# Optimization experiments

Hardware: AMD Instinct MI355X
Metric: run time of the kernel (lower is better)

## Reference

```python
import jax, jax.numpy as jnp
import numpy as np

D_MODEL = 512
NHEAD = 8
HEAD_DIM = D_MODEL // NHEAD
DFF = 2048
KSIZE = 3
EPS = 1e-5


def conv1d(x, w, b, pad):
    # x: [B, Cin, S], w: [Cout, Cin, K] -> [B, Cout, S]
    y = jax.lax.conv_general_dilated(x, w, window_strides=(1,), padding=[(pad, pad)],
                                     dimension_numbers=("NCH", "OIH", "NCH"))
    return y + b[None, :, None]


def layernorm(x, g, b):
    mu = jnp.mean(x, axis=-1, keepdims=True)
    var = jnp.mean(jnp.square(x - mu), axis=-1, keepdims=True)
    return (x - mu) * jax.lax.rsqrt(var + EPS) * g + b


def setup_inputs() -> dict:
    key = jax.random.key(0)
    ks = jax.random.split(key, 16)
    B, S = 8, 1024
    # conv init: normal(0, sqrt(2/(K*out_ch))) per head (out_ch = HEAD_DIM), bias 0.1
    sq = np.sqrt(2.0 / (KSIZE * HEAD_DIM)).astype(np.float32)
    sv = np.sqrt(2.0 / (1 * HEAD_DIM)).astype(np.float32)
    inp = {
        "src": jax.random.normal(ks[0], (B, S, D_MODEL), jnp.float32),
        "Wq": jax.random.normal(ks[1], (D_MODEL, D_MODEL, KSIZE), jnp.float32) * sq,
        "bq": jnp.full((D_MODEL,), 0.1, jnp.float32),
        "Wk": jax.random.normal(ks[2], (D_MODEL, D_MODEL, KSIZE), jnp.float32) * sq,
        "bk": jnp.full((D_MODEL,), 0.1, jnp.float32),
        "Wv": jax.random.normal(ks[3], (D_MODEL, D_MODEL, 1), jnp.float32) * sv,
        "bv": jnp.full((D_MODEL,), 0.1, jnp.float32),
        "Wo": jax.random.normal(ks[4], (D_MODEL, D_MODEL), jnp.float32) * 0.02,
        "bo": jnp.zeros((D_MODEL,), jnp.float32),
        "W1": jax.random.normal(ks[5], (DFF, D_MODEL), jnp.float32) * 0.02,
        "b1": jnp.zeros((DFF,), jnp.float32),
        "W2": jax.random.normal(ks[6], (D_MODEL, DFF), jnp.float32) * 0.02,
        "b2": jnp.zeros((D_MODEL,), jnp.float32),
        "g1": jnp.ones((D_MODEL,), jnp.float32),
        "be1": jnp.zeros((D_MODEL,), jnp.float32),
        "g2": jnp.ones((D_MODEL,), jnp.float32),
        "be2": jnp.zeros((D_MODEL,), jnp.float32),
    }
    return inp


def reference(src, Wq, bq, Wk, bk, Wv, bv, Wo, bo, W1, b1, W2, b2, g1, be1, g2, be2):
    B, S, D = src.shape
    H, hd = NHEAD, HEAD_DIM
    xt = jnp.transpose(src, (0, 2, 1))  # [B, D, S]
    # H per-head convs over the same input == one conv with D output channels
    q = conv1d(xt, Wq, bq, (KSIZE - 1) // 2).reshape(B, H, hd, S)
    k = conv1d(xt, Wk, bk, (KSIZE - 1) // 2).reshape(B, H, hd, S)
    v = conv1d(xt, Wv, bv, 0).reshape(B, H, hd, S)
    # NOTE: source divides by head_dim (not sqrt(head_dim))
    scores = jnp.einsum("bhds,bhdt->bhst", q, k) / hd
    att = jax.nn.softmax(scores, axis=-1)  # [B, H, S, S]
    av = jnp.einsum("bhst,bhdt->bhsd", att, v)  # [B, H, S, hd]
    av = jnp.transpose(av, (0, 2, 1, 3)).reshape(B, S, D)
    sa = av @ Wo.T + bo
    x = layernorm(src + sa, g1, be1)  # post-norm (norm_first=False)
    ff = jax.nn.relu(x @ W1.T + b1) @ W2.T + b2
    return layernorm(x + ff, g2, be2)
```

## Files before the change

### kernel.cpp

```cpp
#include <hip/hip_runtime.h>
#include <hip/hip_bf16.h>

using bf16 = __hip_bfloat16;
typedef __attribute__((ext_vector_type(8))) short s8v;
typedef __attribute__((ext_vector_type(4))) short s4v;
typedef __attribute__((ext_vector_type(4))) float f32x4;

#define DEV __device__ __forceinline__

DEV f32x4 mfma16(s8v a, s8v b, f32x4 c) {
    return __builtin_amdgcn_mfma_f32_16x16x32_bf16(a, b, c, 0, 0, 0);
}

DEV void gl_to_lds16(const bf16* g, bf16* l) {
    __builtin_amdgcn_global_load_lds(
        (const __attribute__((address_space(1))) void*)g,
        (__attribute__((address_space(3))) void*)l, 16, 0, 0);
}

DEV unsigned short bfbits(bf16 h) { union { bf16 h; unsigned short u; } c; c.h = h; return c.u; }
DEV unsigned pk2(float a, float b) {
    return (unsigned)bfbits(__float2bfloat16(a)) | ((unsigned)bfbits(__float2bfloat16(b)) << 16);
}
DEV void unpk8(uint4 u, float* x) {
    const unsigned uu[4] = {u.x, u.y, u.z, u.w};
#pragma unroll
    for (int j = 0; j < 4; j++) {
        x[2 * j]     = __uint_as_float(uu[j] << 16);
        x[2 * j + 1] = __uint_as_float(uu[j] & 0xffff0000u);
    }
}

__global__ __launch_bounds__(256)
void convert_all(const float* __restrict__ src, const float* __restrict__ Wv,
                 const float* __restrict__ Wo, const float* __restrict__ W1,
                 const float* __restrict__ W2, bf16* __restrict__ srcb,
                 bf16* __restrict__ Wvb, bf16* __restrict__ Wob, bf16* __restrict__ W1b,
                 bf16* __restrict__ W2b) {
    const long long i4 = ((long long)blockIdx.x * 256 + threadIdx.x) * 4;
    const float* in;
    bf16* outp;
    long long off;
    if (i4 < 4194304)      { in = src; outp = srcb; off = 0; }
    else if (i4 < 4456448) { in = Wv;  outp = Wvb;  off = 4194304; }
    else if (i4 < 4718592) { in = Wo;  outp = Wob;  off = 4456448; }
    else if (i4 < 5767168) { in = W1;  outp = W1b;  off = 4718592; }
    else                   { in = W2;  outp = W2b;  off = 5767168; }
    const long long j = i4 - off;
    const float4 v = *(const float4*)(in + j);
    uint2 o;
    o.x = pk2(v.x, v.y);
    o.y = pk2(v.z, v.w);
    *(uint2*)(outp + j) = o;
}

__global__ __launch_bounds__(256)
void prep_kernel(const float* __restrict__ Wq, const float* __restrict__ Wk,
                 bf16* __restrict__ WqT, bf16* __restrict__ WkT, bf16* __restrict__ zp) {
    const int i = blockIdx.x * 256 + threadIdx.x;
    if (i < 512) zp[i] = __float2bfloat16(0.f);
    const int dk = i >> 18, rem = i & 262143, co = rem >> 9, ci = rem & 511;
    const size_t s = (size_t)co * 1536 + ci * 3 + dk;
    WqT[i] = __float2bfloat16(Wq[s]);
    WkT[i] = __float2bfloat16(Wk[s]);
}

__global__ __launch_bounds__(256)
void conv_qk(const bf16* __restrict__ src, const bf16* __restrict__ WqT,
             const bf16* __restrict__ WkT, const float* __restrict__ bq,
             const float* __restrict__ bk, bf16* __restrict__ Qo, bf16* __restrict__ Ko,
             const bf16* __restrict__ zp) {
    const int z = blockIdx.z, b = z & 7, isK = z >> 3;
    const bf16* WT = isK ? WkT : WqT;
    const float* bias = isK ? bk : bq;
    bf16* out = isK ? Ko : Qo;
    const float qs = isK ? 1.0f : 0.022542109951390054f;
    const bf16* S = src + ((size_t)b << 19);
    const int m0 = blockIdx.x * 128, n0 = blockIdx.y * 128;
    const int tid = threadIdx.x, w = tid >> 6, l = tid & 63;
    const int wm = (w >> 1) << 6, wn = (w & 1) << 6;
    __shared__ __align__(16) bf16 As[4096], Bs[4096];
    f32x4 acc[4][4] = {};
    for (int k0 = 0; k0 < 1536; k0 += 32) {
        const int dk = k0 >> 9, ci0 = k0 & 511;
        if (k0) __syncthreads();
#pragma unroll
        for (int i = 0; i < 2; i++) {
            const int srow = m0 + i * 64 + w * 16 + (l >> 2) - 1 + dk;
            const bf16* ga = (srow >= 0 && srow < 1024)
                                 ? S + (size_t)srow * 512 + ci0 + (l & 3) * 8
                                 : zp + (l & 3) * 8;
            gl_to_lds16(ga, &As[i * 2048 + w * 512]);
            const int co = n0 + i * 64 + w * 16 + (l >> 2);
            gl_to_lds16(WT + ((size_t)dk << 18) + (size_t)co * 512 + ci0 + (l & 3) * 8,
                        &Bs[i * 2048 + w * 512]);
        }
        __syncthreads();
        s8v af[4], bfv[4];
#pragma unroll
        for (int x = 0; x < 4; x++) {
            af[x]  = *(const s8v*)&As[(wm + x * 16 + (l & 15)) * 32 + ((l >> 4) << 3)];
            bfv[x] = *(const s8v*)&Bs[(wn + x * 16 + (l & 15)) * 32 + ((l >> 4) << 3)];
        }
#pragma unroll
        for (int mt = 0; mt < 4; mt++)
#pragma unroll
            for (int nt = 0; nt < 4; nt++) acc[mt][nt] = mfma16(af[mt], bfv[nt], acc[mt][nt]);
    }
#pragma unroll
    for (int nt = 0; nt < 4; nt++) {
        const int co = n0 + wn + nt * 16 + (l & 15);
        const float bn = bias[co];
        const size_t obase = ((size_t)b << 19) + ((size_t)(co >> 6) << 16) + (co & 63);
#pragma unroll
        for (int mt = 0; mt < 4; mt++)
#pragma unroll
            for (int r = 0; r < 4; r++) {
                const int s = m0 + wm + mt * 16 + ((l >> 4) << 2) + r;
                out[obase + (size_t)s * 64] = __float2bfloat16((acc[mt][nt][r] + bn) * qs);
            }
    }
}

template <int EPI>
__global__ __launch_bounds__(256)
void gemm_nt(const bf16* __restrict__ A, const bf16* __restrict__ B,
             const float* __restrict__ bias, void* __restrict__ C, int M, int N, int K,
             int lda, int ldb, int ldc, long long aOff, long long bOff, long long cOff) {
    const int m0 = blockIdx.x * 128, n0 = blockIdx.y * 128, z = blockIdx.z;
    A += (size_t)z * aOff;
    B += (size_t)z * bOff;
    const int tid = threadIdx.x, w = tid >> 6, l = tid & 63;
    const int wm = (w >> 1) << 6, wn = (w & 1) << 6;
    __shared__ __align__(16) bf16 As[4096], Bs[4096];
    f32x4 acc[4][4] = {};
    for (int k0 = 0; k0 < K; k0 += 32) {
        if (k0) __syncthreads();
#pragma unroll
        for (int i = 0; i < 2; i++) {
            gl_to_lds16(A + (size_t)(m0 + i * 64 + w * 16 + (l >> 2)) * lda + k0 + (l & 3) * 8,
                        &As[i * 2048 + w * 512]);
            gl_to_lds16(B + (size_t)(n0 + i * 64 + w * 16 + (l >> 2)) * ldb + k0 + (l & 3) * 8,
                        &Bs[i * 2048 + w * 512]);
        }
        __syncthreads();
        s8v af[4], bfv[4];
#pragma unroll
        for (int x = 0; x < 4; x++) {
            af[x]  = *(const s8v*)&As[(wm + x * 16 + (l & 15)) * 32 + ((l >> 4) << 3)];
            bfv[x] = *(const s8v*)&Bs[(wn + x * 16 + (l & 15)) * 32 + ((l >> 4) << 3)];
        }
#pragma unroll
        for (int mt = 0; mt < 4; mt++)
#pragma unroll
            for (int nt = 0; nt < 4; nt++) acc[mt][nt] = mfma16(af[mt], bfv[nt], acc[mt][nt]);
    }
#pragma unroll
    for (int nt = 0; nt < 4; nt++) {
        const int n = n0 + wn + nt * 16 + (l & 15);
        const float bn = (EPI == 1) ? bias[n] : 0.f;
#pragma unroll
        for (int mt = 0; mt < 4; mt++)
#pragma unroll
            for (int r = 0; r < 4; r++) {
                const int m = m0 + wm + mt * 16 + ((l >> 4) << 2) + r;
                float v = acc[mt][nt][r];
                const size_t off = (size_t)z * cOff + (size_t)m * ldc + n;
                if (EPI == 3) {
                    ((float*)C)[off] = v;
                } else {
                    v += (EPI == 2) ? bias[m] : bn;
                    if (EPI == 1) v = fmaxf(v, 0.f);
                    ((bf16*)C)[off] = __float2bfloat16(v);
                }
            }
    }
}

__global__ __launch_bounds__(256)
void attn_kernel(const bf16* __restrict__ Q, const bf16* __restrict__ K,
                 const bf16* __restrict__ V, bf16* __restrict__ av) {
    const int bh = blockIdx.y, b = bh >> 3, h = bh & 7;
    const bf16* Qp = Q + ((size_t)bh << 16);
    const bf16* Kp = K + ((size_t)bh << 16);
    const bf16* Vp = V + ((size_t)bh << 16);
    const int tid = threadIdx.x, w = tid >> 6, l = tid & 63;
    const int lq = l & 15, quad = l >> 4;
    const int q0 = blockIdx.x * 128 + w * 16;
    __shared__ __align__(16) bf16 Ks[4096], Vs[4096], Ps[8192];
    bf16* Pw0 = &Ps[(w * 2 + 0) * 1024];
    bf16* Pw1 = &Ps[(w * 2 + 1) * 1024];
    const s8v qf00 = *(const s8v*)&Qp[(size_t)(q0 + lq) * 64 + quad * 8];
    const s8v qf01 = *(const s8v*)&Qp[(size_t)(q0 + lq) * 64 + 32 + quad * 8];
    const s8v qf10 = *(const s8v*)&Qp[(size_t)(q0 + 64 + lq) * 64 + quad * 8];
    const s8v qf11 = *(const s8v*)&Qp[(size_t)(q0 + 64 + lq) * 64 + 32 + quad * 8];
    f32x4 o0[4] = {}, o1[4] = {};
    float l0 = 0.f, l1 = 0.f;
    const int sr = tid >> 3;
    const int scb = tid & 7;
    const int swz_st = (scb ^ (sr & 7)) * 8;
    const int rdz0 = (quad ^ (lq & 7)) * 8;
    const int rdz1 = ((quad + 4) ^ (lq & 7)) * 8;
    const int pwz = ((quad >> 1) ^ (lq & 7)) * 8 + (quad & 1) * 4;
    for (int t0 = 0; t0 < 1024; t0 += 64) {
        __syncthreads();
        *(s8v*)&Ks[sr * 64 + swz_st] = *(const s8v*)&Kp[(size_t)(t0 + sr) * 64 + scb * 8];
        *(s8v*)&Ks[(sr + 32) * 64 + swz_st] =
            *(const s8v*)&Kp[(size_t)(t0 + sr + 32) * 64 + scb * 8];
        *(s8v*)&Vs[sr * 64 + swz_st] = *(const s8v*)&Vp[(size_t)sr * 1024 + t0 + scb * 8];
        *(s8v*)&Vs[(sr + 32) * 64 + swz_st] =
            *(const s8v*)&Vp[(size_t)(sr + 32) * 1024 + t0 + scb * 8];
        __syncthreads();
        f32x4 st0[4] = {}, st1[4] = {};
#pragma unroll
        for (int tt = 0; tt < 4; tt++) {
            const int rb = (tt * 16 + lq) * 64;
            const s8v ka0 = *(const s8v*)&Ks[rb + rdz0];
            const s8v ka1 = *(const s8v*)&Ks[rb + rdz1];
            st0[tt] = mfma16(ka0, qf00, st0[tt]);
            st0[tt] = mfma16(ka1, qf01, st0[tt]);
            st1[tt] = mfma16(ka0, qf10, st1[tt]);
            st1[tt] = mfma16(ka1, qf11, st1[tt]);
        }
        float cs0 = 0.f, cs1 = 0.f;
#pragma unroll
        for (int tt = 0; tt < 4; tt++) {
            const float a0 = exp2f(st0[tt][0]), a1 = exp2f(st0[tt][1]);
            const float a2 = exp2f(st0[tt][2]), a3 = exp2f(st0[tt][3]);
            cs0 += (a0 + a1) + (a2 + a3);
            uint2 pkv;
            pkv.x = pk2(a0, a1);
            pkv.y = pk2(a2, a3);
            *(uint2*)&Pw0[lq * 64 + (pwz ^ (tt * 16))] = pkv;
            const float b0 = exp2f(st1[tt][0]), b1 = exp2f(st1[tt][1]);
            const float b2 = exp2f(st1[tt][2]), b3 = exp2f(st1[tt][3]);
            cs1 += (b0 + b1) + (b2 + b3);
            uint2 pkw;
            pkw.x = pk2(b0, b1);
            pkw.y = pk2(b2, b3);
            *(uint2*)&Pw1[lq * 64 + (pwz ^ (tt * 16))] = pkw;
        }
        cs0 += __shfl_xor(cs0, 16);
        cs0 += __shfl_xor(cs0, 32);
        cs1 += __shfl_xor(cs1, 16);
        cs1 += __shfl_xor(cs1, 32);
        l0 += cs0;
        l1 += cs1;
        const s8v pb00 = *(const s8v*)&Pw0[lq * 64 + rdz0];
        const s8v pb01 = *(const s8v*)&Pw0[lq * 64 + rdz1];
        const s8v pb10 = *(const s8v*)&Pw1[lq * 64 + rdz0];
        const s8v pb11 = *(const s8v*)&Pw1[lq * 64 + rdz1];
#pragma unroll
        for (int dt = 0; dt < 4; dt++) {
            const int rb = (dt * 16 + lq) * 64;
            const s8v va0 = *(const s8v*)&Vs[rb + rdz0];
            const s8v va1 = *(const s8v*)&Vs[rb + rdz1];
            o0[dt] = mfma16(va0, pb00, o0[dt]);
            o0[dt] = mfma16(va1, pb01, o0[dt]);
            o1[dt] = mfma16(va0, pb10, o1[dt]);
            o1[dt] = mfma16(va1, pb11, o1[dt]);
        }
    }
    const float i0 = 1.f / l0, i1 = 1.f / l1;
    const size_t rb0 = ((size_t)b * 1024 + q0 + lq) * 512 + h * 64;
    const size_t rb1 = rb0 + (size_t)64 * 512;
#pragma unroll
    for (int dt = 0; dt < 4; dt++) {
        uint2 ov;
        ov.x = pk2(o0[dt][0] * i0, o0[dt][1] * i0);
        ov.y = pk2(o0[dt][2] * i0, o0[dt][3] * i0);
        *(uint2*)&av[rb0 + dt * 16 + quad * 4] = ov;
        uint2 ow;
        ow.x = pk2(o1[dt][0] * i1, o1[dt][1] * i1);
        ow.y = pk2(o1[dt][2] * i1, o1[dt][3] * i1);
        *(uint2*)&av[rb1 + dt * 16 + quad * 4] = ow;
    }
}

template <int MODE>
__global__ __launch_bounds__(256)
void ln_kernel(const void* __restrict__ A, const float* __restrict__ P0,
               const float* __restrict__ P1, const float* __restrict__ bias,
               const float* __restrict__ g, const float* __restrict__ be,
               void* __restrict__ outp) {
    const int w = threadIdx.x >> 6, l = threadIdx.x & 63;
    const size_t row = (size_t)blockIdx.x * 4 + w;
    const size_t base = row * 512 + l * 8;
    float x[8];
    if (MODE == 1) {
        const float4 a0 = *(const float4*)((const float*)A + base);
        const float4 a1 = *(const float4*)((const float*)A + base + 4);
        x[0] = a0.x; x[1] = a0.y; x[2] = a0.z; x[3] = a0.w;
        x[4] = a1.x; x[5] = a1.y; x[6] = a1.z; x[7] = a1.w;
    } else {
        unpk8(*(const uint4*)((const bf16*)A + base), x);
    }
    const float4 p00 = *(const float4*)(P0 + base);
    const float4 p01 = *(const float4*)(P0 + base + 4);
    const float4 p10 = *(const float4*)(P1 + base);
    const float4 p11 = *(const float4*)(P1 + base + 4);
    const float4 bb0 = *(const float4*)(bias + l * 8);
    const float4 bb1 = *(const float4*)(bias + l * 8 + 4);
    x[0] += p00.x + p10.x + bb0.x; x[1] += p00.y + p10.y + bb0.y;
    x[2] += p00.z + p10.z + bb0.z; x[3] += p00.w + p10.w + bb0.w;
    x[4] += p01.x + p11.x + bb1.x; x[5] += p01.y + p11.y + bb1.y;
    x[6] += p01.z + p11.z + bb1.z; x[7] += p01.w + p11.w + bb1.w;
    float s = 0.f, sq = 0.f;
#pragma unroll
    for (int j = 0; j < 8; j++) { s += x[j]; sq += x[j] * x[j]; }
#pragma unroll
    for (int off = 1; off < 64; off <<= 1) {
        s += __shfl_xor(s, off);
        sq += __shfl_xor(sq, off);
    }
    const float mean = s * (1.f / 512.f);
    const float var = sq * (1.f / 512.f) - mean * mean;
    const float rstd = rsqrtf(fmaxf(var, 0.f) + 1e-5f);
    const float4 g0 = *(const float4*)(g + l * 8);
    const float4 g1 = *(const float4*)(g + l * 8 + 4);
    const float4 e0 = *(const float4*)(be + l * 8);
    const float4 e1 = *(const float4*)(be + l * 8 + 4);
    const float gv[8] = {g0.x, g0.y, g0.z, g0.w, g1.x, g1.y, g1.z, g1.w};
    const float ev[8] = {e0.x, e0.y, e0.z, e0.w, e1.x, e1.y, e1.z, e1.w};
    float y[8];
#pragma unroll
    for (int j = 0; j < 8; j++) y[j] = (x[j] - mean) * rstd * gv[j] + ev[j];
    if (MODE == 1) {
        uint4 o;
        o.x = pk2(y[0], y[1]); o.y = pk2(y[2], y[3]);
        o.z = pk2(y[4], y[5]); o.w = pk2(y[6], y[7]);
        *(uint4*)((bf16*)outp + base) = o;
    } else {
        *(float4*)((float*)outp + base)     = make_float4(y[0], y[1], y[2], y[3]);
        *(float4*)((float*)outp + base + 4) = make_float4(y[4], y[5], y[6], y[7]);
    }
}

extern "C" void kernel_launch(void* const* d_in, const int* in_sizes, int n_in, void* d_out,
                              int out_size, void* d_ws, size_t ws_size, hipStream_t stream) {
    const float* src = (const float*)d_in[0];
    const float* Wq = (const float*)d_in[1];
    const float* bq = (const float*)d_in[2];
    const float* Wk = (const float*)d_in[3];
    const float* bk = (const float*)d_in[4];
    const float* Wv = (const float*)d_in[5];
    const float* bv = (const float*)d_in[6];
    const float* Wo = (const float*)d_in[7];
    const float* bo = (const float*)d_in[8];
    const float* W1 = (const float*)d_in[9];
    const float* b1 = (const float*)d_in[10];
    const float* W2 = (const float*)d_in[11];
    const float* b2 = (const float*)d_in[12];
    const float* g1 = (const float*)d_in[13];
    const float* be1 = (const float*)d_in[14];
    const float* g2 = (const float*)d_in[15];
    const float* be2 = (const float*)d_in[16];
    float* out = (float*)d_out;

    char* base = (char*)d_ws;
    bf16* srcb = (bf16*)(base + 0);
    bf16* Qb   = (bf16*)(base + 8388608);
    bf16* Kb   = (bf16*)(base + 16777216);
    bf16* Vb   = (bf16*)(base + 25165824);
    bf16* ff1  = (bf16*)(base + 0);
    bf16* avb  = (bf16*)(base + 33554432);
    bf16* xb   = avb;
    float* saf = (float*)(base + 41943040);
    bf16* WqT  = (bf16*)(base + 75497472);
    bf16* WkT  = (bf16*)(base + 77070336);
    bf16* zp   = (bf16*)(base + 78643200);
    bf16* Wvb  = (bf16*)(base + 78644224);
    bf16* Wob  = (bf16*)(base + 79168512);
    bf16* W1b  = (bf16*)(base + 79692800);
    bf16* W2b  = (bf16*)(base + 81789952);

    convert_all<<<6656, 256, 0, stream>>>(src, Wv, Wo, W1, W2, srcb, Wvb, Wob, W1b, W2b);
    prep_kernel<<<3072, 256, 0, stream>>>(Wq, Wk, WqT, WkT, zp);
    conv_qk<<<dim3(8, 4, 16), 256, 0, stream>>>(srcb, WqT, WkT, bq, bk, Qb, Kb, zp);
    gemm_nt<2><<<dim3(4, 8, 8), 256, 0, stream>>>(Wvb, srcb, bv, Vb, 512, 1024, 512,
                                                  512, 512, 1024, 0, 524288, 524288);
    attn_kernel<<<dim3(8, 64), 256, 0, stream>>>(Qb, Kb, Vb, avb);
    gemm_nt<3><<<dim3(64, 4, 2), 256, 0, stream>>>(avb, Wob, nullptr, saf, 8192, 512, 256,
                                                   512, 512, 512, 256, 256, 4194304LL);
    ln_kernel<1><<<2048, 256, 0, stream>>>(src, saf, saf + 4194304, bo, g1, be1, xb);
    gemm_nt<1><<<dim3(64, 16, 1), 256, 0, stream>>>(xb, W1b, b1, ff1, 8192, 2048, 512,
                                                    512, 512, 2048, 0, 0, 0);
    gemm_nt<3><<<dim3(64, 4, 2), 256, 0, stream>>>(ff1, W2b, nullptr, saf, 8192, 512, 1024,
                                                   2048, 2048, 512, 1024, 1024, 4194304LL);
    ln_kernel<2><<<2048, 256, 0, stream>>>(xb, saf, saf + 4194304, b2, g2, be2, out);
}
```

Baseline: 291.3 us.

## Prefetch K/V tiles into registers and use raw exp2 with truncating packing

The attention kernel now loads the next K/V tile from global memory into registers while the current tile is being computed, so global latency overlaps the MFMA and softmax work. exp2f is replaced by the hardware exp2 builtin, and bf16 packing switches from round-to-nearest to truncation to save ALU work. The grid is also transposed so that blockIdx.x indexes batch-head, which changes block scheduling order and L2 locality. Truncating the probabilities slightly changes numerics, and the prefetch raises register pressure.

```diff
diff --git a/kernel.cpp b/kernel.cpp
--- a/kernel.cpp
+++ b/kernel.cpp
@@ -21,6 +21,9 @@
 DEV unsigned short bfbits(bf16 h) { union { bf16 h; unsigned short u; } c; c.h = h; return c.u; }
 DEV unsigned pk2(float a, float b) {
     return (unsigned)bfbits(__float2bfloat16(a)) | ((unsigned)bfbits(__float2bfloat16(b)) << 16);
+}
+DEV unsigned pk2t(float a, float b) {
+    return (__float_as_uint(a) >> 16) | (__float_as_uint(b) & 0xffff0000u);
 }
 DEV void unpk8(uint4 u, float* x) {
     const unsigned uu[4] = {u.x, u.y, u.z, u.w};
@@ -180,13 +183,13 @@
 __global__ __launch_bounds__(256)
 void attn_kernel(const bf16* __restrict__ Q, const bf16* __restrict__ K,
                  const bf16* __restrict__ V, bf16* __restrict__ av) {
-    const int bh = blockIdx.y, b = bh >> 3, h = bh & 7;
+    const int bh = blockIdx.x, b = bh >> 3, h = bh & 7;
     const bf16* Qp = Q + ((size_t)bh << 16);
     const bf16* Kp = K + ((size_t)bh << 16);
     const bf16* Vp = V + ((size_t)bh << 16);
     const int tid = threadIdx.x, w = tid >> 6, l = tid & 63;
     const int lq = l & 15, quad = l >> 4;
-    const int q0 = blockIdx.x * 128 + w * 16;
+    const int q0 = blockIdx.y * 128 + w * 16;
     __shared__ __align__(16) bf16 Ks[4096], Vs[4096], Ps[8192];
     bf16* Pw0 = &Ps[(w * 2 + 0) * 1024];
     bf16* Pw1 = &Ps[(w * 2 + 1) * 1024];
@@ -202,14 +205,23 @@
     const int rdz0 = (quad ^ (lq & 7)) * 8;
     const int rdz1 = ((quad + 4) ^ (lq & 7)) * 8;
     const int pwz = ((quad >> 1) ^ (lq & 7)) * 8 + (quad & 1) * 4;
+    s8v kA = *(const s8v*)&Kp[(size_t)sr * 64 + scb * 8];
+    s8v kB = *(const s8v*)&Kp[(size_t)(sr + 32) * 64 + scb * 8];
+    s8v vA = *(const s8v*)&Vp[(size_t)sr * 1024 + scb * 8];
+    s8v vB = *(const s8v*)&Vp[(size_t)(sr + 32) * 1024 + scb * 8];
     for (int t0 = 0; t0 < 1024; t0 += 64) {
         __syncthreads();
-        *(s8v*)&Ks[sr * 64 + swz_st] = *(const s8v*)&Kp[(size_t)(t0 + sr) * 64 + scb * 8];
-        *(s8v*)&Ks[(sr + 32) * 64 + swz_st] =
-            *(const s8v*)&Kp[(size_t)(t0 + sr + 32) * 64 + scb * 8];
-        *(s8v*)&Vs[sr * 64 + swz_st] = *(const s8v*)&Vp[(size_t)sr * 1024 + t0 + scb * 8];
-        *(s8v*)&Vs[(sr + 32) * 64 + swz_st] =
-            *(const s8v*)&Vp[(size_t)(sr + 32) * 1024 + t0 + scb * 8];
+        *(s8v*)&Ks[sr * 64 + swz_st] = kA;
+        *(s8v*)&Ks[(sr + 32) * 64 + swz_st] = kB;
+        *(s8v*)&Vs[sr * 64 + swz_st] = vA;
+        *(s8v*)&Vs[(sr + 32) * 64 + swz_st] = vB;
+        if (t0 + 64 < 1024) {
+            const int t1 = t0 + 64;
+            kA = *(const s8v*)&Kp[(size_t)(t1 + sr) * 64 + scb * 8];
+            kB = *(const s8v*)&Kp[(size_t)(t1 + sr + 32) * 64 + scb * 8];
+            vA = *(const s8v*)&Vp[(size_t)sr * 1024 + t1 + scb * 8];
+            vB = *(const s8v*)&Vp[(size_t)(sr + 32) * 1024 + t1 + scb * 8];
+        }
         __syncthreads();
         f32x4 st0[4] = {}, st1[4] = {};
 #pragma unroll
@@ -225,19 +237,23 @@
         float cs0 = 0.f, cs1 = 0.f;
 #pragma unroll
         for (int tt = 0; tt < 4; tt++) {
-            const float a0 = exp2f(st0[tt][0]), a1 = exp2f(st0[tt][1]);
-            const float a2 = exp2f(st0[tt][2]), a3 = exp2f(st0[tt][3]);
+            const float a0 = __builtin_amdgcn_exp2f(st0[tt][0]);
+            const float a1 = __builtin_amdgcn_exp2f(st0[tt][1]);
+            const float a2 = __builtin_amdgcn_exp2f(st0[tt][2]);
+            const float a3 = __builtin_amdgcn_exp2f(st0[tt][3]);
             cs0 += (a0 + a1) + (a2 + a3);
             uint2 pkv;
-            pkv.x = pk2(a0, a1);
-            pkv.y = pk2(a2, a3);
+            pkv.x = pk2t(a0, a1);
+            pkv.y = pk2t(a2, a3);
             *(uint2*)&Pw0[lq * 64 + (pwz ^ (tt * 16))] = pkv;
-            const float b0 = exp2f(st1[tt][0]), b1 = exp2f(st1[tt][1]);
-            const float b2 = exp2f(st1[tt][2]), b3 = exp2f(st1[tt][3]);
+            const float b0 = __builtin_amdgcn_exp2f(st1[tt][0]);
+            const float b1 = __builtin_amdgcn_exp2f(st1[tt][1]);
+            const float b2 = __builtin_amdgcn_exp2f(st1[tt][2]);
+            const float b3 = __builtin_amdgcn_exp2f(st1[tt][3]);
             cs1 += (b0 + b1) + (b2 + b3);
             uint2 pkw;
-            pkw.x = pk2(b0, b1);
-            pkw.y = pk2(b2, b3);
+            pkw.x = pk2t(b0, b1);
+            pkw.y = pk2t(b2, b3);
             *(uint2*)&Pw1[lq * 64 + (pwz ^ (tt * 16))] = pkw;
         }
         cs0 += __shfl_xor(cs0, 16);
@@ -379,7 +395,7 @@
     conv_qk<<<dim3(8, 4, 16), 256, 0, stream>>>(srcb, WqT, WkT, bq, bk, Qb, Kb, zp);
     gemm_nt<2><<<dim3(4, 8, 8), 256, 0, stream>>>(Wvb, srcb, bv, Vb, 512, 1024, 512,
                                                   512, 512, 1024, 0, 524288, 524288);
-    attn_kernel<<<dim3(8, 64), 256, 0, stream>>>(Qb, Kb, Vb, avb);
+    attn_kernel<<<dim3(64, 8), 256, 0, stream>>>(Qb, Kb, Vb, avb);
     gemm_nt<3><<<dim3(64, 4, 2), 256, 0, stream>>>(avb, Wob, nullptr, saf, 8192, 512, 256,
                                                    512, 512, 512, 256, 256, 4194304LL);
     ln_kernel<1><<<2048, 256, 0, stream>>>(src, saf, saf + 4194304, bo, g1, be1, xb);
```

New measurement: 276.5 us. 5.1% less time.
